# Kernel tuning notes

Measured on AMD Instinct MI355X. Metric: run time of the kernel, lower is better.

Reference implementation:

```python
import jax, jax.numpy as jnp
import numpy as np
import math

FACTOR = 5  # args.factor


def setup_inputs() -> dict:
    key = jax.random.key(0)
    kq, kk, kv, ki = jax.random.split(key, 4)
    B, L, H, D = 8, 2048, 8, 64
    sample_k = min(FACTOR * int(np.ceil(np.log(L))), L)  # 40
    return {
        "queries": jax.random.normal(kq, (B, L, H, D), dtype=jnp.float32),
        "keys": jax.random.normal(kk, (B, L, H, D), dtype=jnp.float32),
        "values": jax.random.normal(kv, (B, L, H, D), dtype=jnp.float32),
        "index_sample": jax.random.randint(ki, (L, sample_k), 0, L),
    }


def reference(queries, keys, values, index_sample):
    B, L_Q, H, D = queries.shape
    L_K = keys.shape[1]
    # [B, L, H, D] -> [B, H, L, D]
    Q = queries.transpose(0, 2, 1, 3)
    K = keys.transpose(0, 2, 1, 3)
    V = values.transpose(0, 2, 1, 3)

    u = min(FACTOR * int(np.ceil(np.log(L_Q))), L_Q)  # n_top

    # ---- _prob_QK: sampled scores + sparsity measure + top-u queries ----
    # gather sampled keys per query position: [B, H, L_Q, sample_k, D]
    K_sample = K[:, :, index_sample, :]
    Q_K_sample = jnp.einsum('bhqd,bhqsd->bhqs', Q, K_sample)  # [B,H,L_Q,S]
    M = Q_K_sample.max(-1) - Q_K_sample.mean(-1)              # [B,H,L_Q]
    _, M_top = jax.lax.top_k(M, u)                            # [B,H,u]

    Q_reduce = jnp.take_along_axis(Q, M_top[..., None], axis=2)  # [B,H,u,D]
    scores = jnp.einsum('bhud,bhkd->bhuk', Q_reduce, K) * (1.0 / math.sqrt(D))

    # ---- initial context: mean of V broadcast over queries ----
    context = jnp.broadcast_to(V.mean(axis=2, keepdims=True), (B, H, L_Q, D))

    # ---- update context at selected query positions ----
    attn = jax.nn.softmax(scores, axis=-1)                  # [B,H,u,L_K]
    ctx_upd = jnp.einsum('bhuk,bhkd->bhud', attn, V)        # [B,H,u,D]
    bi = jnp.arange(B)[:, None, None]
    hi = jnp.arange(H)[None, :, None]
    context = context.at[bi, hi, M_top].set(ctx_upd)

    # [B,H,L_Q,D] -> [B,L_Q,H*D]
    return context.transpose(0, 2, 1, 3).reshape(B, L_Q, H * D)
```

## Files before the change

### kernel.cpp

```cpp
#include <hip/hip_runtime.h>
#include <hip/hip_bf16.h>

#define BB 8
#define LL 2048
#define HH 8
#define DD 64
#define HD 512
#define SK 40
#define UU 40
#define NCHUNK 16
#define CHUNK 128

typedef float v4f __attribute__((ext_vector_type(4)));

static const size_t OFF_M     = 0;
static const size_t OFF_TOP   = 512ull * 1024;
static const size_t OFF_VPART = 592ull * 1024;
static const size_t OFF_MPART = 768ull * 1024;
static const size_t OFF_SPART = 960ull * 1024;
static const size_t OFF_OPART = 1152ull * 1024;

template <int CTRL>
__device__ __forceinline__ float dpp_add(float x) {
    int yi = __builtin_amdgcn_mov_dpp(__float_as_int(x), CTRL, 0xF, 0xF, true);
    return x + __int_as_float(yi);
}

__global__ __launch_bounds__(128) void kA_sample_scores(
    const float* __restrict__ Q, const float* __restrict__ K,
    const int* __restrict__ IS, float* __restrict__ M)
{
    int blk = blockIdx.x;
    int b = blk & 7;
    int q = blk >> 3;
    int tid = threadIdx.x;
    int h = tid >> 4;
    int lane = tid & 15;

    const int* __restrict__ isq = IS + q * SK;
    size_t base = (size_t)b * LL * HD;
    int off = h * DD + lane * 4;
    v4f qv = __builtin_nontemporal_load(
        (const v4f*)(Q + base + (size_t)q * HD + off));
    const float* __restrict__ Kb = K + base;

    float mx = -1e30f, sm = 0.f;
#pragma unroll 8
    for (int s = 0; s < SK; ++s) {
        int idx = __builtin_amdgcn_readfirstlane(isq[s]);
        const float* __restrict__ Krow = Kb + (size_t)idx * HD;
        const float4 kv = *(const float4*)(Krow + off);
        float p = qv.x * kv.x + qv.y * kv.y + qv.z * kv.z + qv.w * kv.w;
        p = dpp_add<0xB1>(p);
        p = dpp_add<0x4E>(p);
        p = dpp_add<0x141>(p);
        p = dpp_add<0x140>(p);
        mx = fmaxf(mx, p);
        sm += p;
    }
    if (lane == 0)
        M[((size_t)(b * HH + h)) * LL + q] = mx - sm * (1.0f / SK);
}

__global__ __launch_bounds__(256) void kB_topk(
    const float* __restrict__ M, int* __restrict__ TopIdx)
{
    int bh = blockIdx.x;
    int tid = threadIdx.x;
    __shared__ unsigned keys[LL];
    __shared__ int      hist[4096];
    __shared__ int      sscan[256];
    __shared__ unsigned ckeyA[2048];
    __shared__ int      cidxA[2048];
    __shared__ unsigned ckeyB[2048];
    __shared__ int      cidxB[2048];
    __shared__ int ctr[8];

    const float* __restrict__ m = M + (size_t)bh * LL;
    for (int i = tid; i < 4096; i += 256) hist[i] = 0;
    if (tid < 8) ctr[tid] = 0;
    __syncthreads();

    for (int i = tid; i < LL; i += 256) {
        unsigned u = __float_as_uint(m[i]);
        u = (u & 0x80000000u) ? ~u : (u | 0x80000000u);
        keys[i] = u;
        atomicAdd(&hist[u >> 20], 1);
    }
    __syncthreads();
    {
        int p = 0;
#pragma unroll
        for (int j = 0; j < 16; ++j) p += hist[tid * 16 + j];
        sscan[tid] = p;
        __syncthreads();
        for (int o = 1; o < 256; o <<= 1) {
            int v = (tid + o < 256) ? sscan[tid + o] : 0;
            __syncthreads();
            sscan[tid] += v;
            __syncthreads();
        }
        int snext = (tid < 255) ? sscan[tid + 1] : 0;
        if (sscan[tid] >= UU && snext < UU) {
            int cum = snext;
            for (int bkt = tid * 16 + 15; bkt >= tid * 16; --bkt) {
                int c = hist[bkt];
                if (cum + c >= UU) { ctr[3] = bkt; ctr[4] = UU - cum; break; }
                cum += c;
            }
        }
    }
    __syncthreads();
    unsigned T1 = (unsigned)ctr[3];
    int k1 = ctr[4];
    for (int i = tid; i < LL; i += 256) {
        unsigned u = keys[i];
        unsigned bkt = u >> 20;
        if (bkt > T1) {
            int p = atomicAdd(&ctr[0], 1);
            TopIdx[bh * UU + p] = i;
        } else if (bkt == T1) {
            int p = atomicAdd(&ctr[1], 1);
            ckeyA[p] = u; cidxA[p] = i;
        }
    }
    __syncthreads();
    int nA = ctr[1];

    for (int i = tid; i < 4096; i += 256) hist[i] = 0;
    __syncthreads();
    for (int i = tid; i < nA; i += 256)
        atomicAdd(&hist[(ckeyA[i] >> 8) & 0xFFF], 1);
    __syncthreads();
    {
        int p = 0;
#pragma unroll
        for (int j = 0; j < 16; ++j) p += hist[tid * 16 + j];
        sscan[tid] = p;
        __syncthreads();
        for (int o = 1; o < 256; o <<= 1) {
            int v = (tid + o < 256) ? sscan[tid + o] : 0;
            __syncthreads();
            sscan[tid] += v;
            __syncthreads();
        }
        int snext = (tid < 255) ? sscan[tid + 1] : 0;
        if (sscan[tid] >= k1 && snext < k1) {
            int cum = snext;
            for (int bkt = tid * 16 + 15; bkt >= tid * 16; --bkt) {
                int c = hist[bkt];
                if (cum + c >= k1) { ctr[3] = bkt; ctr[4] = k1 - cum; break; }
                cum += c;
            }
        }
    }
    __syncthreads();
    unsigned T2 = (unsigned)ctr[3];
    int k2 = ctr[4];
    for (int i = tid; i < nA; i += 256) {
        unsigned u = ckeyA[i];
        unsigned bkt = (u >> 8) & 0xFFF;
        if (bkt > T2) {
            int p = atomicAdd(&ctr[0], 1);
            TopIdx[bh * UU + p] = cidxA[i];
        } else if (bkt == T2) {
            int p = atomicAdd(&ctr[2], 1);
            ckeyB[p] = u; cidxB[p] = cidxA[i];
        }
    }
    __syncthreads();
    int nB = ctr[2];

    for (int i = tid; i < 256; i += 256) hist[i] = 0;
    __syncthreads();
    for (int i = tid; i < nB; i += 256)
        atomicAdd(&hist[ckeyB[i] & 0xFF], 1);
    __syncthreads();
    {
        sscan[tid] = hist[tid];
        __syncthreads();
        for (int o = 1; o < 256; o <<= 1) {
            int v = (tid + o < 256) ? sscan[tid + o] : 0;
            __syncthreads();
            sscan[tid] += v;
            __syncthreads();
        }
        int snext = (tid < 255) ? sscan[tid + 1] : 0;
        if (sscan[tid] >= k2 && snext < k2) { ctr[3] = tid; ctr[4] = k2 - snext; }
    }
    __syncthreads();
    unsigned T3 = (unsigned)ctr[3];
    int k3 = ctr[4];
    for (int i = tid; i < nB; i += 256) {
        unsigned u = ckeyB[i];
        unsigned bkt = u & 0xFF;
        if (bkt > T3) {
            int p = atomicAdd(&ctr[0], 1);
            TopIdx[bh * UU + p] = cidxB[i];
        } else if (bkt == T3) {
            int p = atomicAdd(&ctr[5], 1);
            cidxA[p] = cidxB[i];
        }
    }
    __syncthreads();
    if (tid == 0) {
        int n = ctr[5];
        int basep = ctr[0];
        for (int r = 0; r < k3; ++r) {
            int bi = 1 << 30, bp = -1;
            for (int j = 0; j < n; ++j) {
                int id = cidxA[j];
                if (id >= 0 && id < bi) { bi = id; bp = j; }
            }
            TopIdx[bh * UU + basep + r] = bi;
            cidxA[bp] = -1;
        }
    }
}

__global__ __launch_bounds__(256) void kC_vmean(
    const float* __restrict__ V, float* __restrict__ Vpart)
{
    int bh = blockIdx.x >> 3;
    int ch = blockIdx.x & 7;
    int b = bh >> 3, h = bh & 7;
    int tid = threadIdx.x;
    int dq = tid & 15;
    int lg = tid >> 4;

    float4 acc = make_float4(0.f, 0.f, 0.f, 0.f);
    size_t base = ((size_t)b * LL + ch * 256) * HD + h * DD + dq * 4;
    for (int l = lg; l < 256; l += 16) {
        float4 v = *(const float4*)(V + base + (size_t)l * HD);
        acc.x += v.x; acc.y += v.y; acc.z += v.z; acc.w += v.w;
    }
    __shared__ float4 red[256];
    red[tid] = acc;
    __syncthreads();
    if (tid < 16) {
        float4 s = make_float4(0.f, 0.f, 0.f, 0.f);
#pragma unroll
        for (int g = 0; g < 16; ++g) {
            float4 v = red[g * 16 + tid];
            s.x += v.x; s.y += v.y; s.z += v.z; s.w += v.w;
        }
        *(float4*)(Vpart + ch * 4096 + bh * 64 + tid * 4) = s;
    }
}

__global__ __launch_bounds__(256) void kD_fill(
    const float* __restrict__ Vpart, float* __restrict__ out)
{
    size_t i4 = (size_t)blockIdx.x * 256 + threadIdx.x;
    size_t o = i4 * 4;
    int hd = (int)(o & (HD - 1));
    int b  = (int)(o >> 20);
    int h  = hd >> 6;
    int idx = (b * HH + h) * DD + (hd & 63);
    float4 acc = make_float4(0.f, 0.f, 0.f, 0.f);
#pragma unroll
    for (int c = 0; c < 8; ++c) {
        float4 v = *(const float4*)(Vpart + c * 4096 + idx);
        acc.x += v.x; acc.y += v.y; acc.z += v.z; acc.w += v.w;
    }
    const float sc = 1.0f / LL;
    float4 r; r.x = acc.x * sc; r.y = acc.y * sc; r.z = acc.z * sc; r.w = acc.w * sc;
    *(float4*)(out + o) = r;
}

__global__ __launch_bounds__(256) void kE_attn_partial(
    const float* __restrict__ Q, const float* __restrict__ K, const float* __restrict__ V,
    const int* __restrict__ TopIdx,
    float* __restrict__ Opart, float* __restrict__ mpart, float* __restrict__ spart)
{
    int c  = blockIdx.x;
    int bh = blockIdx.y;
    int b = bh >> 3, h = bh & 7;
    int tid = threadIdx.x;

    __shared__ float Qs[UU * DD];
    __shared__ float P[CHUNK * 41];
    __shared__ int   qidx[UU];
    __shared__ float mred[UU], sred[UU];

    if (tid < UU) qidx[tid] = TopIdx[bh * UU + tid];
    __syncthreads();

    size_t hbase  = (size_t)b * LL * HD + h * DD;
    size_t kcbase = hbase + (size_t)c * CHUNK * HD;

    for (int r = tid; r < UU * 16; r += 256) {
        int u = r >> 4, j = r & 15;
        *(float4*)(Qs + u * DD + j * 4) =
            *(const float4*)(Q + hbase + (size_t)qidx[u] * HD + j * 4);
    }
    __syncthreads();

    {
        int l = tid & (CHUNK - 1), ug = tid >> 7;
        const float* __restrict__ Krow = K + kcbase + (size_t)l * HD;
        float dot[20];
#pragma unroll
        for (int i = 0; i < 20; ++i) dot[i] = 0.f;

#pragma unroll
        for (int half = 0; half < 2; ++half) {
            float4 kr[8];
#pragma unroll
            for (int j = 0; j < 8; ++j)
                kr[j] = *(const float4*)(Krow + half * 32 + j * 4);
#pragma unroll
            for (int j = 0; j < 8; ++j) {
                float4 kv = kr[j];
#pragma unroll
                for (int uu = 0; uu < 20; ++uu) {
                    float4 qv = *(const float4*)(Qs + (ug * 20 + uu) * DD + half * 32 + j * 4);
                    dot[uu] += kv.x * qv.x + kv.y * qv.y + kv.z * qv.z + kv.w * qv.w;
                }
            }
        }
#pragma unroll
        for (int uu = 0; uu < 20; ++uu)
            P[l * 41 + ug * 20 + uu] = dot[uu] * 0.125f;
    }
    __syncthreads();

    if (tid < UU * 4) {
        int u = tid >> 2, part = tid & 3;
        float m = -1e30f;
        for (int l = part * 32; l < part * 32 + 32; ++l) m = fmaxf(m, P[l * 41 + u]);
        m = fmaxf(m, __shfl_xor(m, 1));
        m = fmaxf(m, __shfl_xor(m, 2));
        if (part == 0) mred[u] = m;
    }
    __syncthreads();
    if (tid < UU * 4) {
        int u = tid >> 2, part = tid & 3;
        float m = mred[u];
        float s = 0.f;
        for (int l = part * 32; l < part * 32 + 32; ++l) {
            float p = __expf(P[l * 41 + u] - m);
            P[l * 41 + u] = p;
            s += p;
        }
        s += __shfl_xor(s, 1);
        s += __shfl_xor(s, 2);
        if (part == 0) sred[u] = s;
    }
    __syncthreads();

    {
        int dq = tid & 15, ug4 = tid >> 4;
        float4 acc[3];
#pragma unroll
        for (int i = 0; i < 3; ++i) acc[i] = make_float4(0.f, 0.f, 0.f, 0.f);
        const float* __restrict__ Vb = V + kcbase + dq * 4;
        for (int l0 = 0; l0 < CHUNK; l0 += 8) {
            float4 v[8];
#pragma unroll
            for (int j = 0; j < 8; ++j)
                v[j] = *(const float4*)(Vb + (size_t)(l0 + j) * HD);
#pragma unroll
            for (int j = 0; j < 8; ++j) {
#pragma unroll
                for (int i = 0; i < 3; ++i) {
                    int u = ug4 + 16 * i;
                    if (u < UU) {
                        float p = P[(l0 + j) * 41 + u];
                        acc[i].x += p * v[j].x; acc[i].y += p * v[j].y;
                        acc[i].z += p * v[j].z; acc[i].w += p * v[j].w;
                    }
                }
            }
        }
#pragma unroll
        for (int i = 0; i < 3; ++i) {
            int u = ug4 + 16 * i;
            if (u < UU) {
                size_t ob = (((size_t)(bh * UU + u)) * NCHUNK + c) * DD + dq * 4;
                *(float4*)(Opart + ob) = acc[i];
            }
        }
    }
    if (tid < UU) {
        mpart[(bh * UU + tid) * NCHUNK + c] = mred[tid];
        spart[(bh * UU + tid) * NCHUNK + c] = sred[tid];
    }
}

__global__ __launch_bounds__(64) void kF_combine(
    const float* __restrict__ Opart, const float* __restrict__ mpart,
    const float* __restrict__ spart, const int* __restrict__ TopIdx,
    float* __restrict__ out)
{
    int g = blockIdx.x;
    int bh = g / UU;
    int b = bh >> 3, h = bh & 7;
    int d = threadIdx.x;

    float m_i[NCHUNK];
    float Mx = -1e30f;
#pragma unroll
    for (int i = 0; i < NCHUNK; ++i) { m_i[i] = mpart[g * NCHUNK + i]; Mx = fmaxf(Mx, m_i[i]); }
    float S = 0.f, O = 0.f;
#pragma unroll
    for (int i = 0; i < NCHUNK; ++i) {
        float w = __expf(m_i[i] - Mx);
        S += w * spart[g * NCHUNK + i];
        O += w * Opart[((size_t)g * NCHUNK + i) * DD + d];
    }
    int qi = TopIdx[g];
    out[((size_t)b * LL + qi) * HD + h * DD + d] = O / S;
}

extern "C" void kernel_launch(void* const* d_in, const int* in_sizes, int n_in,
                              void* d_out, int out_size, void* d_ws, size_t ws_size,
                              hipStream_t stream) {
    const float* Q  = (const float*)d_in[0];
    const float* K  = (const float*)d_in[1];
    const float* V  = (const float*)d_in[2];
    const int*   IS = (const int*)d_in[3];
    float* out = (float*)d_out;
    char* ws = (char*)d_ws;

    float* M      = (float*)(ws + OFF_M);
    int*   TopIdx = (int*)(ws + OFF_TOP);
    float* Vpart  = (float*)(ws + OFF_VPART);
    float* mpart  = (float*)(ws + OFF_MPART);
    float* spart  = (float*)(ws + OFF_SPART);
    float* Opart  = (float*)(ws + OFF_OPART);

    kA_sample_scores<<<BB * LL, 128, 0, stream>>>(Q, K, IS, M);
    kC_vmean<<<BB * HH * 8, 256, 0, stream>>>(V, Vpart);
    kB_topk<<<BB * HH, 256, 0, stream>>>(M, TopIdx);
    kD_fill<<<(BB * LL * HD) / (256 * 4), 256, 0, stream>>>(Vpart, out);
    kE_attn_partial<<<dim3(NCHUNK, BB * HH), 256, 0, stream>>>(Q, K, V, TopIdx,
                                                               Opart, mpart, spart);
    kF_combine<<<BB * HH * UU, 64, 0, stream>>>(Opart, mpart, spart, TopIdx, out);
}
```

Baseline: 263.5 us.

## Fuse chunk softmax into score pass with wave DPP reductions, transpose P layout

In the chunked attention kernel, each wave now computes scores for 10 queries over two sets of 64 keys. It performs the max, exp and sum for each query with DPP wave reductions directly in registers, which removes two block barriers and the serial per-thread softmax loops over shared memory. The P buffer is transposed to query-major order with stride 132, so the PV accumulation can read eight probabilities as two float4 shared loads. This adds register pressure from the two K-row sets and the reduction code.

Result: slower. 371.4 us (+40.9%).

```diff
diff --git a/kernel.cpp b/kernel.cpp
--- a/kernel.cpp
+++ b/kernel.cpp
@@ -10,6 +10,7 @@
 #define UU 40
 #define NCHUNK 16
 #define CHUNK 128
+#define PSTR 132
 
 typedef float v4f __attribute__((ext_vector_type(4)));
 
@@ -24,6 +25,36 @@
 __device__ __forceinline__ float dpp_add(float x) {
     int yi = __builtin_amdgcn_mov_dpp(__float_as_int(x), CTRL, 0xF, 0xF, true);
     return x + __int_as_float(yi);
+}
+template <int CTRL>
+__device__ __forceinline__ float dpp_max_step(float x) {
+    int yi = __builtin_amdgcn_update_dpp(__float_as_int(x), __float_as_int(x),
+                                         CTRL, 0xF, 0xF, false);
+    return fmaxf(x, __int_as_float(yi));
+}
+template <int CTRL>
+__device__ __forceinline__ float dpp_sum_step(float x) {
+    int yi = __builtin_amdgcn_update_dpp(0, __float_as_int(x),
+                                         CTRL, 0xF, 0xF, false);
+    return x + __int_as_float(yi);
+}
+__device__ __forceinline__ float wave_max64(float x) {
+    x = dpp_max_step<0xB1>(x);
+    x = dpp_max_step<0x4E>(x);
+    x = dpp_max_step<0x141>(x);
+    x = dpp_max_step<0x140>(x);
+    x = dpp_max_step<0x142>(x);
+    x = dpp_max_step<0x143>(x);
+    return __int_as_float(__builtin_amdgcn_readlane(__float_as_int(x), 63));
+}
+__device__ __forceinline__ float wave_sum64(float x) {
+    x = dpp_sum_step<0xB1>(x);
+    x = dpp_sum_step<0x4E>(x);
+    x = dpp_sum_step<0x141>(x);
+    x = dpp_sum_step<0x140>(x);
+    x = dpp_sum_step<0x142>(x);
+    x = dpp_sum_step<0x143>(x);
+    return __int_as_float(__builtin_amdgcn_readlane(__float_as_int(x), 63));
 }
 
 __global__ __launch_bounds__(128) void kA_sample_scores(
@@ -279,7 +310,7 @@
     int tid = threadIdx.x;
 
     __shared__ float Qs[UU * DD];
-    __shared__ float P[CHUNK * 41];
+    __shared__ float P[UU * PSTR];
     __shared__ int   qidx[UU];
     __shared__ float mred[UU], sred[UU];
 
@@ -297,55 +328,47 @@
     __syncthreads();
 
     {
-        int l = tid & (CHUNK - 1), ug = tid >> 7;
-        const float* __restrict__ Krow = K + kcbase + (size_t)l * HD;
-        float dot[20];
-#pragma unroll
-        for (int i = 0; i < 20; ++i) dot[i] = 0.f;
+        int lt = tid & 63;
+        int ug = tid >> 6;
+        const float* __restrict__ Krow0 = K + kcbase + (size_t)lt * HD;
+        const float* __restrict__ Krow1 = Krow0 + 64 * HD;
+        float dot0[10], dot1[10];
+#pragma unroll
+        for (int i = 0; i < 10; ++i) { dot0[i] = 0.f; dot1[i] = 0.f; }
 
 #pragma unroll
         for (int half = 0; half < 2; ++half) {
-            float4 kr[8];
-#pragma unroll
-            for (int j = 0; j < 8; ++j)
-                kr[j] = *(const float4*)(Krow + half * 32 + j * 4);
+            float4 kr0[8], kr1[8];
 #pragma unroll
             for (int j = 0; j < 8; ++j) {
-                float4 kv = kr[j];
-#pragma unroll
-                for (int uu = 0; uu < 20; ++uu) {
-                    float4 qv = *(const float4*)(Qs + (ug * 20 + uu) * DD + half * 32 + j * 4);
-                    dot[uu] += kv.x * qv.x + kv.y * qv.y + kv.z * qv.z + kv.w * qv.w;
+                kr0[j] = *(const float4*)(Krow0 + half * 32 + j * 4);
+                kr1[j] = *(const float4*)(Krow1 + half * 32 + j * 4);
+            }
+#pragma unroll
+            for (int j = 0; j < 8; ++j) {
+                float4 k0 = kr0[j], k1 = kr1[j];
+#pragma unroll
+                for (int uu = 0; uu < 10; ++uu) {
+                    float4 qv = *(const float4*)(Qs + (ug * 10 + uu) * DD + half * 32 + j * 4);
+                    dot0[uu] += k0.x * qv.x + k0.y * qv.y + k0.z * qv.z + k0.w * qv.w;
+                    dot1[uu] += k1.x * qv.x + k1.y * qv.y + k1.z * qv.z + k1.w * qv.w;
                 }
             }
         }
-#pragma unroll
-        for (int uu = 0; uu < 20; ++uu)
-            P[l * 41 + ug * 20 + uu] = dot[uu] * 0.125f;
-    }
-    __syncthreads();
-
-    if (tid < UU * 4) {
-        int u = tid >> 2, part = tid & 3;
-        float m = -1e30f;
-        for (int l = part * 32; l < part * 32 + 32; ++l) m = fmaxf(m, P[l * 41 + u]);
-        m = fmaxf(m, __shfl_xor(m, 1));
-        m = fmaxf(m, __shfl_xor(m, 2));
-        if (part == 0) mred[u] = m;
-    }
-    __syncthreads();
-    if (tid < UU * 4) {
-        int u = tid >> 2, part = tid & 3;
-        float m = mred[u];
-        float s = 0.f;
-        for (int l = part * 32; l < part * 32 + 32; ++l) {
-            float p = __expf(P[l * 41 + u] - m);
-            P[l * 41 + u] = p;
-            s += p;
-        }
-        s += __shfl_xor(s, 1);
-        s += __shfl_xor(s, 2);
-        if (part == 0) sred[u] = s;
+
+#pragma unroll
+        for (int uu = 0; uu < 10; ++uu) {
+            int u = ug * 10 + uu;
+            float d0 = dot0[uu] * 0.125f;
+            float d1 = dot1[uu] * 0.125f;
+            float m = wave_max64(fmaxf(d0, d1));
+            float p0 = __expf(d0 - m);
+            float p1 = __expf(d1 - m);
+            P[u * PSTR + lt]      = p0;
+            P[u * PSTR + lt + 64] = p1;
+            float s = wave_sum64(p0 + p1);
+            if (lt == 0) { mred[u] = m; sred[u] = s; }
+        }
     }
     __syncthreads();
 
@@ -361,15 +384,27 @@
             for (int j = 0; j < 8; ++j)
                 v[j] = *(const float4*)(Vb + (size_t)(l0 + j) * HD);
 #pragma unroll
-            for (int j = 0; j < 8; ++j) {
-#pragma unroll
-                for (int i = 0; i < 3; ++i) {
-                    int u = ug4 + 16 * i;
-                    if (u < UU) {
-                        float p = P[(l0 + j) * 41 + u];
-                        acc[i].x += p * v[j].x; acc[i].y += p * v[j].y;
-                        acc[i].z += p * v[j].z; acc[i].w += p * v[j].w;
-                    }
+            for (int i = 0; i < 3; ++i) {
+                int u = ug4 + 16 * i;
+                if (u < UU) {
+                    float4 pa = *(const float4*)(P + u * PSTR + l0);
+                    float4 pb = *(const float4*)(P + u * PSTR + l0 + 4);
+                    acc[i].x += pa.x * v[0].x; acc[i].y += pa.x * v[0].y;
+                    acc[i].z += pa.x * v[0].z; acc[i].w += pa.x * v[0].w;
+                    acc[i].x += pa.y * v[1].x; acc[i].y += pa.y * v[1].y;
+                    acc[i].z += pa.y * v[1].z; acc[i].w += pa.y * v[1].w;
+                    acc[i].x += pa.z * v[2].x; acc[i].y += pa.z * v[2].y;
+                    acc[i].z += pa.z * v[2].z; acc[i].w += pa.z * v[2].w;
+                    acc[i].x += pa.w * v[3].x; acc[i].y += pa.w * v[3].y;
+                    acc[i].z += pa.w * v[3].z; acc[i].w += pa.w * v[3].w;
+                    acc[i].x += pb.x * v[4].x; acc[i].y += pb.x * v[4].y;
+                    acc[i].z += pb.x * v[4].z; acc[i].w += pb.x * v[4].w;
+                    acc[i].x += pb.y * v[5].x; acc[i].y += pb.y * v[5].y;
+                    acc[i].z += pb.y * v[5].z; acc[i].w += pb.y * v[5].w;
+                    acc[i].x += pb.z * v[6].x; acc[i].y += pb.z * v[6].y;
+                    acc[i].z += pb.z * v[6].z; acc[i].w += pb.z * v[6].w;
+                    acc[i].x += pb.w * v[7].x; acc[i].y += pb.w * v[7].y;
+                    acc[i].z += pb.w * v[7].z; acc[i].w += pb.w * v[7].w;
                 }
             }
         }
```
